# Kernel optimization log

Measured on AMD Instinct MI355X. Metric: run time of the kernel, lower is better.

## Reference

```python
import jax, jax.numpy as jnp
from jax import lax
import numpy as np

IOU_TH = 0.5
SCORE_TH = 0.05
MAX_PER_CLASS = 10
MAX_TOTAL = 10
K_PRE = 200  # pre-NMS candidates per class (>> max_output_size_per_class)


def make_anchors(image_size: int) -> jnp.ndarray:
    """Replicates AnchorBoxes.create_anchors_boxes for square images (static shapes)."""
    aspect_ratios = [0.5, 1.0, 2.0]
    scales = [2.0 ** 0, 2.0 ** (1.0 / 3.0), 2.0 ** (2.0 / 3.0)]
    step = (image_size - 32) // 4
    areas = [(x * step + 32) ** 2 for x in range(5)]
    strides = [2 ** i for i in range(3, 8)]
    levels = []
    for l in range(5):
        fs = int(np.ceil(image_size / strides[l]))
        dims = []
        for r in aspect_ratios:  # order matches TF code: ratio outer, scale inner
            h = np.sqrt(areas[l] / r)
            w = areas[l] / h
            for s in scales:
                dims.append([s * w, s * h])
        dims = np.asarray(dims, np.float32)  # [9, 2]
        c = (np.arange(fs, dtype=np.float32) + 0.5) * strides[l]
        X, Y = np.meshgrid(c, c)  # 'xy' indexing, as in tf.meshgrid default
        centers = np.stack([X, Y], -1)  # [fs, fs, 2] (cx, cy)
        centers = np.broadcast_to(centers[:, :, None, :], (fs, fs, 9, 2))
        d = np.broadcast_to(dims[None, None], (fs, fs, 9, 2))
        levels.append(np.concatenate([centers, d], -1).reshape(-1, 4))
    return jnp.asarray(np.concatenate(levels, 0))  # [N, 4] (cx, cy, w, h)


def pairwise_iou(b):  # b: [..., K, 4] in corner format
    lt = jnp.maximum(b[..., :, None, :2], b[..., None, :, :2])
    rb = jnp.minimum(b[..., :, None, 2:], b[..., None, :, 2:])
    wh = jnp.clip(rb - lt, 0.0)
    inter = wh[..., 0] * wh[..., 1]
    area = (b[..., 2] - b[..., 0]) * (b[..., 3] - b[..., 1])
    union = area[..., :, None] + area[..., None, :] - inter
    return inter / jnp.maximum(union, 1e-8)


def setup_inputs() -> dict:
    key = jax.random.key(0)
    k1, k2 = jax.random.split(key)
    images = jax.random.normal(k1, (32, 512, 512, 3), dtype=jnp.float32)
    predictions = jax.random.normal(k2, (32, 49104, 7), dtype=jnp.float32)
    return {"images": images, "predictions": predictions}


def reference(images, predictions):
    B = predictions.shape[0]
    anchors = make_anchors(images.shape[1])  # [N, 4], static shape
    box_var = jnp.asarray([0.1, 0.1, 0.2, 0.2], predictions.dtype)

    # Decode boxes.
    bp = predictions[:, :, :4] * box_var
    cls = jax.nn.sigmoid(predictions[:, :, 4:])  # [B, N, C]
    a = anchors[None]
    xy = bp[..., :2] * a[..., 2:] + a[..., :2]
    wh = jnp.exp(bp[..., 2:]) * a[..., 2:]
    boxes = jnp.concatenate([xy - wh / 2.0, xy + wh / 2.0], -1)  # [B, N, 4] corners

    # Combined NMS (class-aware, shared boxes q=1).
    scores = jnp.transpose(cls, (0, 2, 1))  # [B, C, N]
    C = scores.shape[1]
    top_s, top_i = lax.top_k(scores, K_PRE)  # [B, C, K]
    bK = jnp.take_along_axis(boxes[:, None], top_i[..., None], axis=2)  # [B, C, K, 4]
    iou = pairwise_iou(bK)  # [B, C, K, K]
    valid = top_s >= SCORE_TH
    idx = jnp.arange(K_PRE)

    def body(i, keep):
        alive = keep[..., i][..., None]
        suppress = (iou[..., i, :] > IOU_TH) & alive & (idx > i)
        return keep & ~suppress

    keep = lax.fori_loop(0, K_PRE, body, valid)
    sel = jnp.where(keep, top_s, -1.0)

    pc_s, pc_i = lax.top_k(sel, MAX_PER_CLASS)  # [B, C, 10]
    pc_b = jnp.take_along_axis(bK, pc_i[..., None], axis=2)  # [B, C, 10, 4]
    pc_c = jnp.broadcast_to(jnp.arange(C, dtype=jnp.float32)[None, :, None], pc_s.shape)

    flat_s = pc_s.reshape(B, -1)
    flat_b = pc_b.reshape(B, -1, 4)
    flat_c = pc_c.reshape(B, -1)
    fs, fi = lax.top_k(flat_s, MAX_TOTAL)  # [B, 10]
    fb = jnp.take_along_axis(flat_b, fi[..., None], axis=1)
    fc = jnp.take_along_axis(flat_c, fi, axis=1)

    valid_mask = fs > 0.0
    nmsed_boxes = jnp.where(valid_mask[..., None], fb, 0.0)
    nmsed_scores = jnp.where(valid_mask, fs, 0.0)
    nmsed_classes = jnp.where(valid_mask, fc, 0.0)
    valid_detections = jnp.sum(valid_mask, axis=-1).astype(jnp.int32)
    return nmsed_boxes, nmsed_scores, nmsed_classes, valid_detections
```

## Files before the change

kernel.cpp:

```cpp
#include <hip/hip_runtime.h>
#include <math.h>

#define NA     49104
#define NB     32
#define KPRE   200
#define CAP    2048
#define NSLICE 64
#define NQ4    85932
#define PERQ   1344
#define STHR   448
#define TAU    2.0f
#define NBINS  512
#define SSLOT  96

#define CSTRIDE   16
#define WS_COUNT  0
#define WS_KEYS   6144
#define WS_S10    (WS_KEYS + 96*CAP*8)
#define WS_B10    (WS_S10 + 3840)
#define WS_ZERO_U32 (96*CSTRIDE)

__device__ __forceinline__ void anchor_of(int idx, float& cx, float& cy,
                                          float& aw, float& ah) {
    int l, r;
    if (idx < 36864)      { l = 0; r = idx; }
    else if (idx < 46080) { l = 1; r = idx - 36864; }
    else if (idx < 48384) { l = 2; r = idx - 46080; }
    else if (idx < 48960) { l = 3; r = idx - 48384; }
    else                  { l = 4; r = idx - 48960; }
    const int   fss[5]     = {64, 32, 16, 8, 4};
    const int   strides[5] = {8, 16, 32, 64, 128};
    const double areas[5]  = {1024.0, 23104.0, 73984.0, 153664.0, 262144.0};
    int a    = r % 9;
    int cell = r / 9;
    int fs   = fss[l];
    int jx   = cell % fs;
    int iy   = cell / fs;
    cx = ((float)jx + 0.5f) * (float)strides[l];
    cy = ((float)iy + 0.5f) * (float)strides[l];
    int ri = a / 3, si = a % 3;
    double ratio = (ri == 0) ? 0.5 : ((ri == 1) ? 1.0 : 2.0);
    double h = sqrt(areas[l] / ratio);
    double w = areas[l] / h;
    double s = (si == 0) ? 1.0
             : ((si == 1) ? 1.2599210498948732
                          : 1.5874010519681994);
    aw = (float)(s * w);
    ah = (float)(s * h);
}

__device__ __forceinline__ int bin_of(float x) {
    int bin = (int)floorf((x + 8.0f) * 32.0f);
    return min(max(bin, 0), NBINS - 1);
}

__device__ __forceinline__ unsigned omap(float x) {
    unsigned u = __float_as_uint(x);
    return u ^ ((u >> 31) ? 0xFFFFFFFFu : 0x80000000u);
}

__global__ __launch_bounds__(256) void zero_kernel(unsigned* __restrict__ p) {
    int i = blockIdx.x * 256 + threadIdx.x;
    if (i < WS_ZERO_U32) p[i] = 0u;
}

__global__ __launch_bounds__(STHR) void scan_kernel(
        const float* __restrict__ pred, unsigned* __restrict__ count,
        unsigned long long* __restrict__ keys) {
    const int blk = blockIdx.x;
    const int b   = blk >> 6;
    const int sl  = blk & 63;
    const int tid = threadIdx.x;

    __shared__ unsigned long long stage[3][SSLOT];
    __shared__ unsigned scnt[3];
    __shared__ unsigned sbase[3];
    if (tid < 3) scnt[tid] = 0u;
    __syncthreads();

    const int p = tid % 7;
    int cls[4];
    #pragma unroll
    for (int j = 0; j < 4; ++j) {
        int f = (4 * p + j) % 7;
        cls[j] = (f >= 4) ? (f - 4) : -1;
    }

    const float4* row = (const float4*)(pred + (size_t)b * NA * 7);
    const int q0 = sl * PERQ + tid;
    const int q1 = q0 + STHR, q2 = q1 + STHR;
    float4 v0, v1, v2;
    bool g0 = q0 < NQ4, g1 = q1 < NQ4, g2 = q2 < NQ4;
    if (g0) v0 = row[q0];
    if (g1) v1 = row[q1];
    if (g2) v2 = row[q2];

    #pragma unroll
    for (int it = 0; it < 3; ++it) {
        bool   g = (it == 0) ? g0 : (it == 1) ? g1 : g2;
        float4 v = (it == 0) ? v0 : (it == 1) ? v1 : v2;
        int    q = (it == 0) ? q0 : (it == 1) ? q1 : q2;
        if (!g) continue;
        float vv[4] = {v.x, v.y, v.z, v.w};
        #pragma unroll
        for (int j = 0; j < 4; ++j) {
            if (cls[j] >= 0 && vv[j] >= TAU) {
                int e = (q << 2) + j;
                int n = e / 7;
                unsigned u = __float_as_uint(vv[j]) | 0x80000000u;
                unsigned long long key =
                    ((unsigned long long)(~u) << 32) | (unsigned)n;
                int c = cls[j];
                unsigned pos = atomicAdd(&scnt[c], 1u);
                if (pos < SSLOT) stage[c][pos] = key;
                else {
                    unsigned gp = atomicAdd(&count[(b*3+c) * CSTRIDE], 1u);
                    if (gp < CAP) keys[(size_t)(b*3+c) * CAP + gp] = key;
                }
            }
        }
    }
    __syncthreads();

    if (tid < 3) {
        unsigned n = min(scnt[tid], (unsigned)SSLOT);
        sbase[tid] = atomicAdd(&count[(b*3+tid) * CSTRIDE], n);
    }
    __syncthreads();
    #pragma unroll
    for (int c = 0; c < 3; ++c) {
        unsigned n    = min(scnt[c], (unsigned)SSLOT);
        unsigned base = sbase[c];
        for (unsigned i = tid; i < n; i += STHR) {
            unsigned pp = base + i;
            if (pp < CAP) keys[(size_t)(b*3+c) * CAP + pp] = stage[c][i];
        }
    }
}

__device__ __forceinline__ void bitonic_sort(unsigned long long* buf, unsigned P,
                                             int tid) {
    for (unsigned k = 2; k <= P; k <<= 1) {
        for (unsigned j = k >> 1; j > 0; j >>= 1) {
            for (unsigned i = tid; i < P; i += 256) {
                unsigned ixj = i ^ j;
                if (ixj > i) {
                    bool up = ((i & k) == 0);
                    unsigned long long a = buf[i], bb = buf[ixj];
                    if ((a > bb) == up) { buf[i] = bb; buf[ixj] = a; }
                }
            }
            __syncthreads();
        }
    }
}

__global__ __launch_bounds__(256) void nms_kernel(
        const float* __restrict__ pred, const unsigned* __restrict__ count,
        const unsigned long long* __restrict__ gkeys,
        float* __restrict__ s10, float4* __restrict__ b10) {
    const int blk = blockIdx.x;
    const int b   = blk / 3;
    const int c   = blk % 3;
    const int tid = threadIdx.x;

    __shared__ unsigned long long keybuf[CAP];
    __shared__ unsigned long long sortbuf[512];
    __shared__ float4 boxes[KPRE];
    __shared__ float  scores_s[256];
    __shared__ unsigned long long mask[256][4];
    __shared__ unsigned hist[256];
    __shared__ unsigned hist512[NBINS];
    __shared__ unsigned sMn[4], sMx[4];
    __shared__ unsigned sel_thr, sel_cnt, s_prefB, s_cumB, s_M, s_sh;
    __shared__ int sT;

    unsigned cnt = count[blk * CSTRIDE];
    if (cnt >= KPRE && cnt <= CAP) {
        unsigned M = min(cnt, (unsigned)CAP);
        for (int i = tid; i < CAP; i += 256)
            keybuf[i] = (i < (int)M) ? gkeys[(size_t)blk * CAP + i] : ~0ULL;
        if (tid == 0) s_M = M;
    } else {
        for (int i = tid; i < NBINS; i += 256) hist512[i] = 0u;
        for (int i = tid; i < CAP;   i += 256) keybuf[i] = ~0ULL;
        if (tid == 0) s_M = 0u;
        __syncthreads();
        const float* base = pred + (size_t)b * NA * 7 + 4 + c;
        for (int n = tid; n < NA; n += 256)
            atomicAdd(&hist512[bin_of(base[(size_t)n * 7])], 1u);
        __syncthreads();
        if (tid < 64) {
            unsigned h[8]; unsigned lsum = 0;
            #pragma unroll
            for (int k = 0; k < 8; ++k) { h[k] = hist512[tid*8+k]; lsum += h[k]; }
            unsigned suf = lsum;
            #pragma unroll
            for (int off = 1; off < 64; off <<= 1) {
                unsigned v = __shfl_down(suf, off, 64);
                if (tid < 64 - off) suf += v;
            }
            unsigned acc = suf - lsum;
            #pragma unroll
            for (int k = 7; k >= 0; --k) {
                unsigned na = acc + h[k];
                if (na >= KPRE && acc < KPRE) sT = max(tid*8 + k - 1, 0);
                acc = na;
            }
        }
        __syncthreads();
        const int T = sT;
        for (int n = tid; n < NA; n += 256) {
            float x = base[(size_t)n * 7];
            if (bin_of(x) >= T) {
                unsigned long long key =
                    ((unsigned long long)(~omap(x)) << 32) | (unsigned)n;
                unsigned pos = atomicAdd(&s_M, 1u);
                if (pos < CAP) keybuf[pos] = key;
            }
        }
    }
    for (int i = tid; i < 512; i += 256) sortbuf[i] = ~0ULL;
    for (int i = tid; i < 256; i += 256) hist[i] = 0u;
    if (tid == 0) sel_cnt = 0u;
    __syncthreads();
    const unsigned M = min(s_M, (unsigned)CAP);

    if (M > KPRE) {
        {
            unsigned mn = 0xFFu, mx = 0u;
            for (int i = tid; i < (int)M; i += 256) {
                unsigned h = (unsigned)(keybuf[i] >> 56);
                mn = min(mn, h); mx = max(mx, h);
            }
            #pragma unroll
            for (int off = 1; off < 64; off <<= 1) {
                mn = min(mn, (unsigned)__shfl_xor((int)mn, off, 64));
                mx = max(mx, (unsigned)__shfl_xor((int)mx, off, 64));
            }
            if ((tid & 63) == 0) { sMn[tid >> 6] = mn; sMx[tid >> 6] = mx; }
        }
        __syncthreads();
        if (tid == 0) {
            unsigned mn = min(min(sMn[0], sMn[1]), min(sMn[2], sMn[3]));
            unsigned mx = max(max(sMx[0], sMx[1]), max(sMx[2], sMx[3]));
            s_sh = (mn == mx) ? 40u : 48u;
        }
        __syncthreads();
        const unsigned sh = s_sh;

        for (int i = tid; i < (int)M; i += 256)
            atomicAdd(&hist[(unsigned)(keybuf[i] >> (sh + 8)) & 0xFFu], 1u);
        __syncthreads();
        if (tid < 64) {
            unsigned h0 = hist[tid*4],   h1 = hist[tid*4+1];
            unsigned h2 = hist[tid*4+2], h3 = hist[tid*4+3];
            unsigned lsum = h0 + h1 + h2 + h3;
            unsigned pre = lsum;
            #pragma unroll
            for (int off = 1; off < 64; off <<= 1) {
                unsigned v = __shfl_up(pre, off, 64);
                if (tid >= off) pre += v;
            }
            unsigned acc = pre - lsum;
            if (acc < KPRE) {
                if      (acc + h0            >= KPRE) { s_prefB = tid*4;   s_cumB = acc; }
                else if (acc + h0 + h1       >= KPRE) { s_prefB = tid*4+1; s_cumB = acc+h0; }
                else if (acc + h0 + h1 + h2  >= KPRE) { s_prefB = tid*4+2; s_cumB = acc+h0+h1; }
                else if (acc + lsum          >= KPRE) { s_prefB = tid*4+3; s_cumB = acc+h0+h1+h2; }
            }
        }
        __syncthreads();
        const unsigned B = s_prefB, before = s_cumB;
        for (int i = tid; i < 256; i += 256) hist[i] = 0u;
        __syncthreads();
        for (int i = tid; i < (int)M; i += 256) {
            unsigned long long key = keybuf[i];
            if (((unsigned)(key >> (sh + 8)) & 0xFFu) == B)
                atomicAdd(&hist[(unsigned)(key >> sh) & 0xFFu], 1u);
        }
        __syncthreads();
        if (tid < 64) {
            const unsigned target = KPRE - before;
            unsigned h0 = hist[tid*4],   h1 = hist[tid*4+1];
            unsigned h2 = hist[tid*4+2], h3 = hist[tid*4+3];
            unsigned lsum = h0 + h1 + h2 + h3;
            unsigned pre = lsum;
            #pragma unroll
            for (int off = 1; off < 64; off <<= 1) {
                unsigned v = __shfl_up(pre, off, 64);
                if (tid >= off) pre += v;
            }
            unsigned acc = pre - lsum;
            if (acc < target) {
                unsigned b2 = 256;
                if      (acc + h0           >= target) b2 = tid*4;
                else if (acc + h0 + h1      >= target) b2 = tid*4+1;
                else if (acc + h0 + h1 + h2 >= target) b2 = tid*4+2;
                else if (acc + lsum         >= target) b2 = tid*4+3;
                if (b2 < 256) sel_thr = (B << 8) | b2;
            }
        }
        __syncthreads();
        const unsigned thr = sel_thr;
        for (int i = tid; i < (int)M; i += 256) {
            unsigned long long key = keybuf[i];
            if (((unsigned)(key >> sh) & 0xFFFFu) <= thr) {
                unsigned pos = atomicAdd(&sel_cnt, 1u);
                if (pos < 512) sortbuf[pos] = key;
            }
        }
        __syncthreads();
    } else {
        for (int i = tid; i < (int)M; i += 256) sortbuf[i] = keybuf[i];
        if (tid == 0) sel_cnt = M;
        __syncthreads();
    }

    unsigned C2 = sel_cnt;
    unsigned long long* sorted;
    if (C2 <= 512) {
        unsigned P = 256; while (P < C2) P <<= 1;
        bitonic_sort(sortbuf, P, tid);
        sorted = sortbuf;
    } else {
        bitonic_sort(keybuf, CAP, tid);
        sorted = keybuf;
    }

    if (tid < KPRE) {
        unsigned long long key = sorted[tid];
        if (key != ~0ULL) {
            unsigned n = (unsigned)key;
            unsigned v = ~(unsigned)(key >> 32);
            v = (v >> 31) ? (v ^ 0x80000000u) : ~v;
            float x  = __uint_as_float(v);
            float sc = 1.0f / (1.0f + expf(-x));
            const float* bp = pred + (size_t)b * NA * 7 + (size_t)n * 7;
            float d0 = bp[0] * 0.1f, d1 = bp[1] * 0.1f;
            float d2 = bp[2] * 0.2f, d3 = bp[3] * 0.2f;
            float cx, cy, aw, ah;
            anchor_of((int)n, cx, cy, aw, ah);
            float xx = d0 * aw + cx;
            float yy = d1 * ah + cy;
            float ww = expf(d2) * aw;
            float hh = expf(d3) * ah;
            boxes[tid]    = make_float4(xx - ww * 0.5f, yy - hh * 0.5f,
                                        xx + ww * 0.5f, yy + hh * 0.5f);
            scores_s[tid] = sc;
        } else {
            boxes[tid]    = make_float4(0, 0, 0, 0);
            scores_s[tid] = -1.0f;
        }
    } else {
        scores_s[tid] = -1.0f;
        mask[tid][0] = 0ULL; mask[tid][1] = 0ULL;
        mask[tid][2] = 0ULL; mask[tid][3] = 0ULL;
    }
    __syncthreads();

    if (tid < KPRE) {
        float4 bi = boxes[tid];
        float areai = (bi.z - bi.x) * (bi.w - bi.y);
        unsigned long long m0 = 0, m1 = 0, m2 = 0, m3 = 0;
#define IOU_CHUNK(MV, LO, HI)                                                  \
        for (int j = (tid + 1 > (LO) ? tid + 1 : (LO)); j < (HI); ++j) {       \
            float4 bj = boxes[j];                                              \
            float x1 = fmaxf(bi.x, bj.x), y1 = fmaxf(bi.y, bj.y);              \
            float x2 = fminf(bi.z, bj.z), y2 = fminf(bi.w, bj.w);              \
            float iw = fmaxf(x2 - x1, 0.0f), ih = fmaxf(y2 - y1, 0.0f);        \
            float inter = iw * ih;                                             \
            float areaj = (bj.z - bj.x) * (bj.w - bj.y);                       \
            float uni   = fmaxf(areai + areaj - inter, 1e-8f);                 \
            if (inter / uni > 0.5f) MV |= 1ULL << (j - (LO));                  \
        }
        IOU_CHUNK(m0,   0,  64)
        IOU_CHUNK(m1,  64, 128)
        IOU_CHUNK(m2, 128, 192)
        IOU_CHUNK(m3, 192, KPRE)
#undef IOU_CHUNK
        mask[tid][0] = m0; mask[tid][1] = m1;
        mask[tid][2] = m2; mask[tid][3] = m3;
    }
    __syncthreads();

    if (tid < 64) {
        const int lane = tid;
        unsigned long long keep[4];
        #pragma unroll
        for (int cb = 0; cb < 4; ++cb)
            keep[cb] = __ballot(scores_s[cb * 64 + lane] >= 0.05f);

        #pragma unroll
        for (int cb = 0; cb < 4; ++cb) {
            unsigned long long mw_self = mask[cb * 64 + lane][cb];
            unsigned long long kw   = keep[cb];
            unsigned long long work = kw & __ballot(mw_self != 0ULL);
            while (work) {
                int t = __ffsll(work) - 1;
                work &= work - 1;
                if ((kw >> t) & 1ULL) {
                    unsigned long long m = __shfl(mw_self, t, 64);
                    kw   &= ~m;
                    work &= ~m;
                }
            }
            keep[cb] = kw;
            #pragma unroll
            for (int w = cb + 1; w < 4; ++w) {
                unsigned long long myw = mask[cb * 64 + lane][w];
                if ((__ballot(myw != 0ULL) & kw) == 0ULL) continue;
                unsigned long long contrib = ((kw >> lane) & 1ULL) ? myw : 0ULL;
                #pragma unroll
                for (int off = 1; off < 64; off <<= 1)
                    contrib |= __shfl_xor(contrib, off, 64);
                keep[w] &= ~contrib;
            }
        }

        if (lane == 0) {
            int k = 0;
            #pragma unroll
            for (int cb = 0; cb < 4; ++cb) {
                unsigned long long kw = keep[cb];
                while (kw && k < 10) {
                    int t = __ffsll(kw) - 1; kw &= kw - 1;
                    int i = cb * 64 + t;
                    s10[blk * 10 + k] = scores_s[i];
                    b10[blk * 10 + k] = boxes[i];
                    ++k;
                }
            }
            #pragma unroll
            for (int cb = 0; cb < 4; ++cb) {
                unsigned long long nk = ~keep[cb];
                if (cb == 3) nk &= 0xFFULL;
                while (nk && k < 10) {
                    int t = __ffsll(nk) - 1; nk &= nk - 1;
                    int i = cb * 64 + t;
                    s10[blk * 10 + k] = -1.0f;
                    b10[blk * 10 + k] = boxes[i];
                    ++k;
                }
            }
        }
    }
}

__global__ __launch_bounds__(64) void merge_kernel(
        const float* __restrict__ s10, const float4* __restrict__ b10,
        float* __restrict__ out) {
    const int b   = blockIdx.x;
    const int tid = threadIdx.x;

    float s = (tid < 30) ? s10[b * 30 + tid] : -2.0f;

    float* ob = out + b * 40;
    float* os = out + 1280 + b * 10;
    float* oc = out + 1600 + b * 10;
    float* ov = out + 1920 + b;

    int valid = 0;
    for (int k = 0; k < 10; ++k) {
        unsigned u = __float_as_uint(s);
        unsigned o = (u >> 31) ? ~u : (u | 0x80000000u);
        unsigned long long key = ((unsigned long long)o << 6) | (unsigned)(63 - tid);
        #pragma unroll
        for (int off = 1; off < 64; off <<= 1) {
            unsigned long long k2 = __shfl_xor(key, off, 64);
            key = (k2 > key) ? k2 : key;
        }
        int t = 63 - (int)(key & 63ULL);
        float best = __shfl(s, t, 64);
        bool v = best > 0.0f;
        if (tid == t) {
            float4 bb = v ? b10[b * 30 + t] : make_float4(0, 0, 0, 0);
            ob[k * 4 + 0] = bb.x; ob[k * 4 + 1] = bb.y;
            ob[k * 4 + 2] = bb.z; ob[k * 4 + 3] = bb.w;
            os[k] = v ? best : 0.0f;
            oc[k] = v ? (float)(t / 10) : 0.0f;
            s = -2.0f;
        }
        valid += v ? 1 : 0;
    }
    if (tid == 0) ov[0] = (float)valid;
}

extern "C" void kernel_launch(void* const* d_in, const int* in_sizes, int n_in,
                              void* d_out, int out_size, void* d_ws, size_t ws_size,
                              hipStream_t stream) {
    const float* pred = (const float*)d_in[1];

    char* ws = (char*)d_ws;
    unsigned*            count = (unsigned*)           (ws + WS_COUNT);
    unsigned long long*  keys  = (unsigned long long*) (ws + WS_KEYS);
    float*               s10   = (float*)              (ws + WS_S10);
    float4*              b10   = (float4*)             (ws + WS_B10);

    zero_kernel <<<(WS_ZERO_U32 + 255) / 256, 256, 0, stream>>>((unsigned*)ws);
    scan_kernel <<<NB * NSLICE, STHR, 0, stream>>>(pred, count, keys);
    nms_kernel  <<<96, 256, 0, stream>>>(pred, count, keys, s10, b10);
    merge_kernel<<<32, 64, 0, stream>>>(s10, b10, (float*)d_out);
}
```

Measured before the change: 66.04 us.

## Drop zero and merge launches via per-slice slots and in-kernel merge handshake

The scan kernel now writes candidate keys into fixed per-slice slots and records per-slice counts, which removes the global atomic counters and the zero-initialisation kernel. The NMS kernel compacts the slots with a wave prefix sum. Extra blocks spin on a per-image done counter and perform the final merge inside the same launch, replacing the separate merge kernel. Small candidate sets are sorted with a register and shuffle bitonic network instead of the shared-memory sort. This cuts two kernel launches and some barriers, at the cost of spin-waiting blocks, which depend on the producer blocks being scheduled first, and a fallback path when any slice overflows.

```diff
diff --git a/kernel.cpp b/kernel.cpp
--- a/kernel.cpp
+++ b/kernel.cpp
@@ -1,24 +1,23 @@
 #include <hip/hip_runtime.h>
 #include <math.h>
 
-#define NA     49104
-#define NB     32
-#define KPRE   200
-#define CAP    2048
-#define NSLICE 64
-#define NQ4    85932
-#define PERQ   1344
-#define STHR   448
-#define TAU    2.0f
-#define NBINS  512
-#define SSLOT  96
-
-#define CSTRIDE   16
-#define WS_COUNT  0
-#define WS_KEYS   6144
-#define WS_S10    (WS_KEYS + 96*CAP*8)
-#define WS_B10    (WS_S10 + 3840)
-#define WS_ZERO_U32 (96*CSTRIDE)
+#define NA      49104
+#define NB      32
+#define KPRE    200
+#define CAP     2048
+#define NSLICE  64
+#define NQ4     85932
+#define PERQ    1344
+#define STHR    448
+#define TAU     2.0f
+#define NBINS   512
+#define SLOTCAP 64
+
+#define WS_CNT   0
+#define WS_KEYS  24576
+#define WS_S10   (WS_KEYS + 96*NSLICE*SLOTCAP*8)
+#define WS_B10   (WS_S10 + 96*10*4)
+#define WS_DONE  (WS_B10 + 96*10*16)
 
 __device__ __forceinline__ void anchor_of(int idx, float& cx, float& cy,
                                           float& aw, float& ah) {
@@ -59,22 +58,24 @@
     return u ^ ((u >> 31) ? 0xFFFFFFFFu : 0x80000000u);
 }
 
-__global__ __launch_bounds__(256) void zero_kernel(unsigned* __restrict__ p) {
-    int i = blockIdx.x * 256 + threadIdx.x;
-    if (i < WS_ZERO_U32) p[i] = 0u;
+__device__ __forceinline__ unsigned long long shfl_xor_u64(unsigned long long v,
+                                                           int m) {
+    unsigned lo = (unsigned)v, hi = (unsigned)(v >> 32);
+    lo = __shfl_xor(lo, m, 64);
+    hi = __shfl_xor(hi, m, 64);
+    return ((unsigned long long)hi << 32) | lo;
 }
 
 __global__ __launch_bounds__(STHR) void scan_kernel(
-        const float* __restrict__ pred, unsigned* __restrict__ count,
-        unsigned long long* __restrict__ keys) {
+        const float* __restrict__ pred, unsigned* __restrict__ cnts,
+        unsigned long long* __restrict__ keys, unsigned* __restrict__ done) {
     const int blk = blockIdx.x;
     const int b   = blk >> 6;
     const int sl  = blk & 63;
     const int tid = threadIdx.x;
 
-    __shared__ unsigned long long stage[3][SSLOT];
+    __shared__ unsigned long long stage[3][SLOTCAP];
     __shared__ unsigned scnt[3];
-    __shared__ unsigned sbase[3];
     if (tid < 3) scnt[tid] = 0u;
     __syncthreads();
 
@@ -112,29 +113,21 @@
                     ((unsigned long long)(~u) << 32) | (unsigned)n;
                 int c = cls[j];
                 unsigned pos = atomicAdd(&scnt[c], 1u);
-                if (pos < SSLOT) stage[c][pos] = key;
-                else {
-                    unsigned gp = atomicAdd(&count[(b*3+c) * CSTRIDE], 1u);
-                    if (gp < CAP) keys[(size_t)(b*3+c) * CAP + gp] = key;
-                }
-            }
-        }
-    }
-    __syncthreads();
-
-    if (tid < 3) {
-        unsigned n = min(scnt[tid], (unsigned)SSLOT);
-        sbase[tid] = atomicAdd(&count[(b*3+tid) * CSTRIDE], n);
-    }
-    __syncthreads();
+                if (pos < SLOTCAP) stage[c][pos] = key;
+            }
+        }
+    }
+    __syncthreads();
+
+    if (tid < 3) cnts[(b * 3 + tid) * NSLICE + sl] = scnt[tid];
+    if (tid == 3 && sl == 0) done[b] = 0u;
+
     #pragma unroll
     for (int c = 0; c < 3; ++c) {
-        unsigned n    = min(scnt[c], (unsigned)SSLOT);
-        unsigned base = sbase[c];
-        for (unsigned i = tid; i < n; i += STHR) {
-            unsigned pp = base + i;
-            if (pp < CAP) keys[(size_t)(b*3+c) * CAP + pp] = stage[c][i];
-        }
+        unsigned n = min(scnt[c], (unsigned)SLOTCAP);
+        unsigned long long* dst =
+            keys + ((size_t)(b * 3 + c) * NSLICE + sl) * SLOTCAP;
+        for (unsigned i = tid; i < n; i += STHR) dst[i] = stage[c][i];
     }
 }
 
@@ -155,14 +148,61 @@
     }
 }
 
-__global__ __launch_bounds__(256) void nms_kernel(
-        const float* __restrict__ pred, const unsigned* __restrict__ count,
+__global__ __launch_bounds__(256) void nms_merge_kernel(
+        const float* __restrict__ pred, const unsigned* __restrict__ cnts,
         const unsigned long long* __restrict__ gkeys,
-        float* __restrict__ s10, float4* __restrict__ b10) {
+        float* __restrict__ s10, float4* __restrict__ b10,
+        unsigned* __restrict__ done, float* __restrict__ out) {
     const int blk = blockIdx.x;
-    const int b   = blk / 3;
-    const int c   = blk % 3;
     const int tid = threadIdx.x;
+
+    if (blk >= 96) {
+        const int b = blk - 96;
+        if (tid == 0) {
+            while (__hip_atomic_load(&done[b], __ATOMIC_ACQUIRE,
+                                     __HIP_MEMORY_SCOPE_AGENT) < 3u)
+                __builtin_amdgcn_s_sleep(8);
+        }
+        __syncthreads();
+        __threadfence();
+
+        if (tid < 64) {
+            float s = (tid < 30) ? s10[b * 30 + tid] : -2.0f;
+            float* ob = out + b * 40;
+            float* os = out + 1280 + b * 10;
+            float* oc = out + 1600 + b * 10;
+            float* ov = out + 1920 + b;
+            int valid = 0;
+            for (int k = 0; k < 10; ++k) {
+                unsigned u = __float_as_uint(s);
+                unsigned o = (u >> 31) ? ~u : (u | 0x80000000u);
+                unsigned long long key =
+                    ((unsigned long long)o << 6) | (unsigned)(63 - tid);
+                #pragma unroll
+                for (int off = 1; off < 64; off <<= 1) {
+                    unsigned long long k2 = __shfl_xor(key, off, 64);
+                    key = (k2 > key) ? k2 : key;
+                }
+                int t = 63 - (int)(key & 63ULL);
+                float best = __shfl(s, t, 64);
+                bool v = best > 0.0f;
+                if (tid == t) {
+                    float4 bb = v ? b10[b * 30 + t] : make_float4(0, 0, 0, 0);
+                    ob[k * 4 + 0] = bb.x; ob[k * 4 + 1] = bb.y;
+                    ob[k * 4 + 2] = bb.z; ob[k * 4 + 3] = bb.w;
+                    os[k] = v ? best : 0.0f;
+                    oc[k] = v ? (float)(t / 10) : 0.0f;
+                    s = -2.0f;
+                }
+                valid += v ? 1 : 0;
+            }
+            if (tid == 0) ov[0] = (float)valid;
+        }
+        return;
+    }
+
+    const int b = blk / 3;
+    const int c = blk % 3;
 
     __shared__ unsigned long long keybuf[CAP];
     __shared__ unsigned long long sortbuf[512];
@@ -171,19 +211,45 @@
     __shared__ unsigned long long mask[256][4];
     __shared__ unsigned hist[256];
     __shared__ unsigned hist512[NBINS];
+    __shared__ unsigned Lb[NSLICE], Bb[NSLICE];
     __shared__ unsigned sMn[4], sMx[4];
-    __shared__ unsigned sel_thr, sel_cnt, s_prefB, s_cumB, s_M, s_sh;
+    __shared__ unsigned sel_thr, sel_cnt, s_prefB, s_cumB, s_M, s_sh, s_common;
     __shared__ int sT;
 
-    unsigned cnt = count[blk * CSTRIDE];
-    if (cnt >= KPRE && cnt <= CAP) {
-        unsigned M = min(cnt, (unsigned)CAP);
-        for (int i = tid; i < CAP; i += 256)
-            keybuf[i] = (i < (int)M) ? gkeys[(size_t)blk * CAP + i] : ~0ULL;
-        if (tid == 0) s_M = M;
+    for (int i = tid; i < CAP; i += 256) keybuf[i] = ~0ULL;
+    for (int i = tid; i < 512; i += 256) sortbuf[i] = ~0ULL;
+    for (int i = tid; i < 256; i += 256) hist[i] = 0u;
+    if (tid == 0) sel_cnt = 0u;
+    __syncthreads();
+
+    if (tid < 64) {
+        unsigned L  = cnts[blk * NSLICE + tid];
+        unsigned Lc = min(L, (unsigned)SLOTCAP);
+        unsigned pre = Lc;
+        #pragma unroll
+        for (int off = 1; off < 64; off <<= 1) {
+            unsigned v = __shfl_up(pre, off, 64);
+            if (tid >= off) pre += v;
+        }
+        Lb[tid] = Lc;
+        Bb[tid] = pre - Lc;
+        unsigned long long ob = __ballot(L > SLOTCAP);
+        if (tid == 63) s_M = pre;
+        if (tid == 0)  s_common = (ob == 0ULL) ? 1u : 0u;
+    }
+    __syncthreads();
+
+    const unsigned M0 = s_M;
+    const bool common = s_common && M0 >= KPRE && M0 <= CAP;
+
+    if (common) {
+        const unsigned long long* src = gkeys + (size_t)blk * NSLICE * SLOTCAP;
+        for (int i = tid; i < NSLICE * SLOTCAP; i += 256) {
+            int sl = i >> 6, k = i & (SLOTCAP - 1);
+            if ((unsigned)k < Lb[sl]) keybuf[Bb[sl] + k] = src[i];
+        }
     } else {
         for (int i = tid; i < NBINS; i += 256) hist512[i] = 0u;
-        for (int i = tid; i < CAP;   i += 256) keybuf[i] = ~0ULL;
         if (tid == 0) s_M = 0u;
         __syncthreads();
         const float* base = pred + (size_t)b * NA * 7 + 4 + c;
@@ -220,9 +286,6 @@
             }
         }
     }
-    for (int i = tid; i < 512; i += 256) sortbuf[i] = ~0ULL;
-    for (int i = tid; i < 256; i += 256) hist[i] = 0u;
-    if (tid == 0) sel_cnt = 0u;
     __syncthreads();
     const unsigned M = min(s_M, (unsigned)CAP);
 
@@ -317,11 +380,52 @@
         __syncthreads();
     }
 
-    unsigned C2 = sel_cnt;
+    const unsigned C2 = sel_cnt;
     unsigned long long* sorted;
-    if (C2 <= 512) {
-        unsigned P = 256; while (P < C2) P <<= 1;
-        bitonic_sort(sortbuf, P, tid);
+    if (C2 <= 256) {
+        unsigned long long v = (tid < (int)C2) ? sortbuf[tid] : ~0ULL;
+        __syncthreads();
+        #pragma unroll
+        for (unsigned k = 2; k <= 64; k <<= 1) {
+            for (unsigned j = k >> 1; j > 0; j >>= 1) {
+                unsigned long long o = shfl_xor_u64(v, (int)j);
+                bool tm = (((tid & k) == 0) == ((tid & j) == 0));
+                v = tm ? (v < o ? v : o) : (v > o ? v : o);
+            }
+        }
+        {
+            sortbuf[tid] = v; __syncthreads();
+            unsigned long long o = sortbuf[tid ^ 64]; __syncthreads();
+            bool tm = (((tid & 128) == 0) == ((tid & 64) == 0));
+            v = tm ? (v < o ? v : o) : (v > o ? v : o);
+            #pragma unroll
+            for (unsigned j = 32; j > 0; j >>= 1) {
+                unsigned long long o2 = shfl_xor_u64(v, (int)j);
+                bool t2 = (((tid & 128) == 0) == ((tid & j) == 0));
+                v = t2 ? (v < o2 ? v : o2) : (v > o2 ? v : o2);
+            }
+        }
+        {
+            sortbuf[tid] = v; __syncthreads();
+            unsigned long long o = sortbuf[tid ^ 128]; __syncthreads();
+            bool tm = ((tid & 128) == 0);
+            v = tm ? (v < o ? v : o) : (v > o ? v : o);
+            sortbuf[tid] = v; __syncthreads();
+            o = sortbuf[tid ^ 64]; __syncthreads();
+            tm = ((tid & 64) == 0);
+            v = tm ? (v < o ? v : o) : (v > o ? v : o);
+            #pragma unroll
+            for (unsigned j = 32; j > 0; j >>= 1) {
+                unsigned long long o2 = shfl_xor_u64(v, (int)j);
+                bool t2 = ((tid & j) == 0);
+                v = t2 ? (v < o2 ? v : o2) : (v > o2 ? v : o2);
+            }
+        }
+        sortbuf[tid] = v;
+        __syncthreads();
+        sorted = sortbuf;
+    } else if (C2 <= 512) {
+        bitonic_sort(sortbuf, 512, tid);
         sorted = sortbuf;
     } else {
         bitonic_sort(keybuf, CAP, tid);
@@ -443,47 +547,11 @@
                     ++k;
                 }
             }
-        }
-    }
-}
-
-__global__ __launch_bounds__(64) void merge_kernel(
-        const float* __restrict__ s10, const float4* __restrict__ b10,
-        float* __restrict__ out) {
-    const int b   = blockIdx.x;
-    const int tid = threadIdx.x;
-
-    float s = (tid < 30) ? s10[b * 30 + tid] : -2.0f;
-
-    float* ob = out + b * 40;
-    float* os = out + 1280 + b * 10;
-    float* oc = out + 1600 + b * 10;
-    float* ov = out + 1920 + b;
-
-    int valid = 0;
-    for (int k = 0; k < 10; ++k) {
-        unsigned u = __float_as_uint(s);
-        unsigned o = (u >> 31) ? ~u : (u | 0x80000000u);
-        unsigned long long key = ((unsigned long long)o << 6) | (unsigned)(63 - tid);
-        #pragma unroll
-        for (int off = 1; off < 64; off <<= 1) {
-            unsigned long long k2 = __shfl_xor(key, off, 64);
-            key = (k2 > key) ? k2 : key;
-        }
-        int t = 63 - (int)(key & 63ULL);
-        float best = __shfl(s, t, 64);
-        bool v = best > 0.0f;
-        if (tid == t) {
-            float4 bb = v ? b10[b * 30 + t] : make_float4(0, 0, 0, 0);
-            ob[k * 4 + 0] = bb.x; ob[k * 4 + 1] = bb.y;
-            ob[k * 4 + 2] = bb.z; ob[k * 4 + 3] = bb.w;
-            os[k] = v ? best : 0.0f;
-            oc[k] = v ? (float)(t / 10) : 0.0f;
-            s = -2.0f;
-        }
-        valid += v ? 1 : 0;
-    }
-    if (tid == 0) ov[0] = (float)valid;
+            __threadfence();
+            __hip_atomic_fetch_add(&done[b], 1u, __ATOMIC_RELEASE,
+                                   __HIP_MEMORY_SCOPE_AGENT);
+        }
+    }
 }
 
 extern "C" void kernel_launch(void* const* d_in, const int* in_sizes, int n_in,
@@ -492,13 +560,13 @@
     const float* pred = (const float*)d_in[1];
 
     char* ws = (char*)d_ws;
-    unsigned*            count = (unsigned*)           (ws + WS_COUNT);
-    unsigned long long*  keys  = (unsigned long long*) (ws + WS_KEYS);
-    float*               s10   = (float*)              (ws + WS_S10);
-    float4*              b10   = (float4*)             (ws + WS_B10);
-
-    zero_kernel <<<(WS_ZERO_U32 + 255) / 256, 256, 0, stream>>>((unsigned*)ws);
-    scan_kernel <<<NB * NSLICE, STHR, 0, stream>>>(pred, count, keys);
-    nms_kernel  <<<96, 256, 0, stream>>>(pred, count, keys, s10, b10);
-    merge_kernel<<<32, 64, 0, stream>>>(s10, b10, (float*)d_out);
-}
+    unsigned*            cnts = (unsigned*)           (ws + WS_CNT);
+    unsigned long long*  keys = (unsigned long long*) (ws + WS_KEYS);
+    float*               s10  = (float*)              (ws + WS_S10);
+    float4*              b10  = (float4*)             (ws + WS_B10);
+    unsigned*            done = (unsigned*)           (ws + WS_DONE);
+
+    scan_kernel     <<<NB * NSLICE, STHR, 0, stream>>>(pred, cnts, keys, done);
+    nms_merge_kernel<<<128, 256, 0, stream>>>(pred, cnts, keys, s10, b10, done,
+                                              (float*)d_out);
+}
```

Measured after the change: 65.07 us. About the same (-1.5%).
